# Kernel tuning notes

Hardware: AMD Instinct MI355X
Metric: run time of the kernel (lower is better)

Reference implementation:

```python
import jax, jax.numpy as jnp
import numpy as np

S, B, D_MODEL, H, DH = 2048, 2, 1024, 16, 64
FACTOR = 1.0 / np.sqrt(DH).astype(np.float32)


def setup_inputs() -> dict:
    key = jax.random.key(0)
    ks = jax.random.split(key, 12)
    sc = 0.02
    inp = {
        'query': jax.random.normal(ks[0], (S, B, D_MODEL), jnp.float32),
        'key': jax.random.normal(ks[1], (S, B, D_MODEL), jnp.float32),
        'value': jax.random.normal(ks[2], (S, B, D_MODEL), jnp.float32),
        # causal mask [seq_q, seq_k, 1]; 0 -> masked
        'mask': jnp.tril(jnp.ones((S, S), dtype=bool))[:, :, None],
        'Wq': jax.random.normal(ks[3], (H * DH, D_MODEL), jnp.float32) * sc,
        'bq': jnp.zeros((H * DH,), jnp.float32),
        'Wk': jax.random.normal(ks[4], (H * DH, D_MODEL), jnp.float32) * sc,
        'bk': jnp.zeros((H * DH,), jnp.float32),
        'Wv': jax.random.normal(ks[5], (H * DH, D_MODEL), jnp.float32) * sc,
        'bv': jnp.zeros((H * DH,), jnp.float32),
        'Wo': jax.random.normal(ks[6], (D_MODEL, H * DH), jnp.float32) * sc,
        'bo': jnp.zeros((D_MODEL,), jnp.float32),
    }
    return inp


def _split_heads(x):
    # pattern: 's b (head_dim head_num) -> s b head_num head_dim' (head_dim is OUTER)
    s, b, _ = x.shape
    return x.reshape(s, b, DH, H).transpose(0, 1, 3, 2)  # [s,b,H,DH]


def reference(query, key, value, mask, Wq, bq, Wk, bk, Wv, bv, Wo, bo):
    q = _split_heads(query @ Wq.T + bq)
    k = _split_heads(key @ Wk.T + bk)
    v = _split_heads(value @ Wv.T + bv)
    scores = jnp.einsum('ibhd,jbhd->ijbh', q, k) * FACTOR  # [i,j,b,h]
    scores = jnp.where(mask[..., None], scores, -jnp.inf)
    attn = jax.nn.softmax(scores, axis=1)  # softmax over keys (dim=1)
    out = jnp.einsum('ijbh,jbhd->ibhd', attn, v)  # [i,b,h,d]
    out = out.reshape(S, B, H * DH)  # 'i b h d -> i b (h d)'
    return out @ Wo.T + bo
```

## Files before the change

### kernel.cpp

```cpp
#include <hip/hip_runtime.h>


typedef float f32x4 __attribute__((ext_vector_type(4)));
typedef float f32x16 __attribute__((ext_vector_type(16)));
typedef __bf16 bf16x8_t __attribute__((ext_vector_type(8)));
typedef unsigned short ushort8 __attribute__((ext_vector_type(8)));
typedef unsigned int uint4v __attribute__((ext_vector_type(4)));
typedef unsigned int uint2v __attribute__((ext_vector_type(2)));

#define S_LEN 2048
#define BATCH 2
#define DMODEL 1024
#define NHEAD 16
#define DHEAD 64
#define K_SCALE 0.18033688011112042f

__device__ __forceinline__ unsigned short f2bf(float x) {
  unsigned int u = __builtin_bit_cast(unsigned int, x);
  u += 0x7fffu + ((u >> 16) & 1u);
  return (unsigned short)(u >> 16);
}

__device__ __forceinline__ f32x4 mfma16(ushort8 a, ushort8 b, f32x4 c) {
  return __builtin_amdgcn_mfma_f32_16x16x32_bf16(
      __builtin_bit_cast(bf16x8_t, a), __builtin_bit_cast(bf16x8_t, b), c, 0, 0, 0);
}
__device__ __forceinline__ f32x16 mfma32(ushort8 a, ushort8 b, f32x16 c) {
  return __builtin_amdgcn_mfma_f32_32x32x16_bf16(
      __builtin_bit_cast(bf16x8_t, a), __builtin_bit_cast(bf16x8_t, b), c, 0, 0, 0);
}

__device__ __forceinline__ ushort8 pack8(float4 a, float4 b, float s) {
  ushort8 t;
  t[0] = f2bf(a.x * s); t[1] = f2bf(a.y * s); t[2] = f2bf(a.z * s); t[3] = f2bf(a.w * s);
  t[4] = f2bf(b.x * s); t[5] = f2bf(b.y * s); t[6] = f2bf(b.z * s); t[7] = f2bf(b.w * s);
  return t;
}

__device__ __forceinline__ void gload16(unsigned short* lds, const unsigned short* g) {
  __builtin_amdgcn_global_load_lds(
      (const __attribute__((address_space(1))) unsigned int*)g,
      (__attribute__((address_space(3))) unsigned int*)lds, 16, 0, 0);
}

__global__ __launch_bounds__(256) void cvt_kernel(
    const float* __restrict__ q, const float* __restrict__ k, const float* __restrict__ v,
    const float* __restrict__ wq, const float* __restrict__ wk,
    const float* __restrict__ wv, const float* __restrict__ wo,
    unsigned short* __restrict__ qB, unsigned short* __restrict__ kB,
    unsigned short* __restrict__ vB, unsigned short* __restrict__ wqB,
    unsigned short* __restrict__ wkB, unsigned short* __restrict__ wvB,
    unsigned short* __restrict__ woB)
{
  const int c = blockIdx.x * 256 + threadIdx.x;
  const float* s; unsigned short* d; int base;
  if      (c < 524288)  { s = q;  d = qB;  base = 0; }
  else if (c < 1048576) { s = k;  d = kB;  base = 524288; }
  else if (c < 1572864) { s = v;  d = vB;  base = 1048576; }
  else if (c < 1703936) { s = wq; d = wqB; base = 1572864; }
  else if (c < 1835008) { s = wk; d = wkB; base = 1703936; }
  else if (c < 1966080) { s = wv; d = wvB; base = 1835008; }
  else                  { s = wo; d = woB; base = 1966080; }
  const size_t off = (size_t)(c - base) * 8;
  const float4 v0 = *reinterpret_cast<const float4*>(s + off);
  const float4 v1 = *reinterpret_cast<const float4*>(s + off + 4);
  *reinterpret_cast<ushort8*>(d + off) = pack8(v0, v1, 1.0f);
}

template<bool OUTBF16>
__global__ __launch_bounds__(256) void gemm_bf16_kernel(
    const unsigned short* __restrict__ A, const unsigned short* __restrict__ W,
    const float* __restrict__ bias, void* __restrict__ Cv, float oscale)
{
  __shared__ __align__(16) unsigned short As[2][128 * 64];
  __shared__ __align__(16) unsigned short Ws[2][64 * 64];
  const int tid = threadIdx.x;
  const int lane = tid & 63;
  const int w = tid >> 6;
  const int wm = (w >> 1) * 64, wn = (w & 1) * 32;
  const int g = lane >> 4, lr = lane & 15;

  const int bid = (int)blockIdx.x;
  const int widx = (bid & 7) * 64 + (bid >> 3);
  const int n0 = (widx & 15) * 64;
  const int m0 = (widx >> 4) * 128;

  f32x4 acc[4][2] = {};

#define STAGE(buf, k0)                                                              \
  {                                                                                 \
    _Pragma("unroll")                                                               \
    for (int ii = 0; ii < 4; ++ii) {                                                \
      const int c = ii * 256 + tid;                                                 \
      const int row = c >> 3;                                                       \
      const int sl = (c & 7) ^ (row & 7);                                           \
      gload16(&As[buf][c * 8], A + (size_t)(m0 + row) * DMODEL + (k0) + sl * 8);    \
    }                                                                               \
    _Pragma("unroll")                                                               \
    for (int ii = 0; ii < 2; ++ii) {                                                \
      const int c = ii * 256 + tid;                                                 \
      const int row = c >> 3;                                                       \
      const int sl = (c & 7) ^ (row & 7);                                           \
      gload16(&Ws[buf][c * 8], W + (size_t)(n0 + row) * DMODEL + (k0) + sl * 8);    \
    }                                                                               \
  }

  STAGE(0, 0);
  int cur = 0;

  for (int t = 0; t < 16; ++t) {
    __syncthreads();
    if (t < 15) STAGE(cur ^ 1, (t + 1) * 64);

    const char* ab = (const char*)&As[cur][0];
    const char* wb = (const char*)&Ws[cur][0];
#pragma unroll
    for (int kk = 0; kk < 2; ++kk) {
      ushort8 af[4], bw[2];
#pragma unroll
      for (int mt = 0; mt < 4; ++mt) {
        const int row = wm + mt * 16 + lr;
        af[mt] = *reinterpret_cast<const ushort8*>(
            ab + row * 128 + (((kk * 4 + g) ^ (row & 7)) << 4));
      }
#pragma unroll
      for (int nt = 0; nt < 2; ++nt) {
        const int row = wn + nt * 16 + lr;
        bw[nt] = *reinterpret_cast<const ushort8*>(
            wb + row * 128 + (((kk * 4 + g) ^ (row & 7)) << 4));
      }
      __builtin_amdgcn_s_setprio(1);
#pragma unroll
      for (int mt = 0; mt < 4; ++mt)
#pragma unroll
        for (int nt = 0; nt < 2; ++nt)
          acc[mt][nt] = mfma16(af[mt], bw[nt], acc[mt][nt]);
      __builtin_amdgcn_s_setprio(0);
    }
    cur ^= 1;
  }
#undef STAGE

#pragma unroll
  for (int nt = 0; nt < 2; ++nt) {
    const int col = n0 + wn + nt * 16 + lr;
    const float bv = bias[col];
#pragma unroll
    for (int mt = 0; mt < 4; ++mt)
#pragma unroll
      for (int r = 0; r < 4; ++r) {
        const int rowg = m0 + wm + mt * 16 + g * 4 + r;
        const float vv = (acc[mt][nt][r] + bv) * oscale;
        if constexpr (OUTBF16)
          ((unsigned short*)Cv)[(size_t)rowg * DMODEL + col] = f2bf(vv);
        else
          ((float*)Cv)[(size_t)rowg * DMODEL + col] = vv;
      }
  }
}

__global__ __launch_bounds__(256) void head_tr0_kernel(
    const unsigned short* __restrict__ in, unsigned short* __restrict__ out)
{
  __shared__ __align__(16) unsigned short T[32 * 256];
  const int tid = threadIdx.x;
  const int n0 = blockIdx.x * 32, o0 = blockIdx.y * 256;
#pragma unroll
  for (int i = 0; i < 4; ++i) {
    const int c = i * 256 + tid;
    const int row = c >> 5, c8 = c & 31;
    ushort8 v = *reinterpret_cast<const ushort8*>(in + (size_t)(n0 + row) * DMODEL + o0 + c8 * 8);
    int y = (row * 512 + c8 * 16) ^ ((row & 3) << 5);
    *reinterpret_cast<ushort8*>((char*)T + y) = v;
  }
  __syncthreads();
  const int d0 = o0 >> 4, s0 = n0 >> 1;
#pragma unroll
  for (int rep = 0; rep < 2; ++rep) {
    const int e = rep * 256 + tid;
    const int hh = e & 15, s = (e >> 4) & 15, b = (e >> 8) & 1;
    const int n = s * 2 + b;
    unsigned short vals[16];
#pragma unroll
    for (int dd = 0; dd < 16; ++dd) {
      int y = n * 512 + ((dd * 32 + hh * 2) ^ ((n & 3) << 5));
      vals[dd] = *(const unsigned short*)((const char*)T + y);
    }
    uint4v w0, w1;
#pragma unroll
    for (int j = 0; j < 4; ++j) {
      w0[j] = (unsigned)vals[2 * j] | ((unsigned)vals[2 * j + 1] << 16);
      w1[j] = (unsigned)vals[8 + 2 * j] | ((unsigned)vals[8 + 2 * j + 1] << 16);
    }
    unsigned short* dst = out + ((size_t)(b * 16 + hh) * S_LEN + s0 + s) * DHEAD + d0;
    *reinterpret_cast<uint4v*>(dst) = w0;
    *reinterpret_cast<uint4v*>(dst + 8) = w1;
  }
}

__global__ __launch_bounds__(256) void head_tr1_kernel(
    const unsigned short* __restrict__ in, unsigned short* __restrict__ out)
{
  __shared__ __align__(16) unsigned short T[64 * 64];
  const int tid = threadIdx.x;
  const int n0 = blockIdx.x * 64, o0 = blockIdx.y * 64;
#pragma unroll
  for (int i = 0; i < 2; ++i) {
    const int c = i * 256 + tid;
    const int row = c >> 3, c8 = c & 7;
    ushort8 v = *reinterpret_cast<const ushort8*>(in + (size_t)(n0 + row) * DMODEL + o0 + c8 * 8);
    int y = (row * 128 + c8 * 16) ^ ((row & 7) << 4);
    *reinterpret_cast<ushort8*>((char*)T + y) = v;
  }
  __syncthreads();
  const int d0 = o0 >> 4, s0 = n0 >> 1;
  const int shalf = tid & 1, seg = tid >> 1;
  const int dd = seg & 3, hh = (seg >> 2) & 15, b = (seg >> 6) & 1;
  unsigned short vals[16];
#pragma unroll
  for (int i = 0; i < 16; ++i) {
    const int s = shalf * 16 + i;
    const int n = s * 2 + b;
    int y = n * 128 + (((dd * 16 + hh) * 2) ^ ((n & 7) << 4));
    vals[i] = *(const unsigned short*)((const char*)T + y);
  }
  uint4v w0, w1;
#pragma unroll
  for (int j = 0; j < 4; ++j) {
    w0[j] = (unsigned)vals[2 * j] | ((unsigned)vals[2 * j + 1] << 16);
    w1[j] = (unsigned)vals[8 + 2 * j] | ((unsigned)vals[8 + 2 * j + 1] << 16);
  }
  unsigned short* dst = out + ((size_t)(b * 16 + hh) * DHEAD + d0 + dd) * S_LEN + s0 + shalf * 16;
  *reinterpret_cast<uint4v*>(dst) = w0;
  *reinterpret_cast<uint4v*>(dst + 8) = w1;
}

__global__ __launch_bounds__(128, 3) void attn_kernel(
    const unsigned short* __restrict__ Qh, const unsigned short* __restrict__ Kh,
    const unsigned short* __restrict__ Vh, unsigned short* __restrict__ O)
{
  __shared__ __align__(16) unsigned short Ks[2][64 * 64];
  __shared__ __align__(16) unsigned short Vs[2][64 * 64];

  const int tid = threadIdx.x;
  const int lane = tid & 63;
  const int w = tid >> 6;
  const int ln31 = lane & 31;
  const int hf = lane >> 5;

  const int bx = blockIdx.x;
  const int hb = bx & 31;
  const int head = hb & 15, b = hb >> 4;
  const int qt = 31 - (bx >> 5);
  const int q0 = qt * 64;
  const int nkt = qt + 1;
  const size_t hoff = (size_t)(b * NHEAD + head) * (S_LEN * DHEAD);
  const unsigned short* Qg = Qh + hoff;
  const unsigned short* Kg = Kh + hoff;
  const unsigned short* Vg = Vh + hoff;

  ushort8 qf[4];
  {
    const int qrow = q0 + w * 32 + ln31;
#pragma unroll
    for (int kt = 0; kt < 4; ++kt)
      qf[kt] = *reinterpret_cast<const ushort8*>(Qg + (size_t)qrow * DHEAD + kt * 16 + hf * 8);
  }

  f32x16 oa0 = {0}, oa1 = {0};
  float mrun = -1e30f, ssum = 0.f;
  const int qg = q0 + w * 32 + ln31;

#define STAGE(buf, kv)                                                             \
  {                                                                                \
    _Pragma("unroll")                                                              \
    for (int ii = 0; ii < 4; ++ii) {                                               \
      const int c = ii * 128 + tid;                                                \
      const int row = c >> 3;                                                      \
      const int sl = (c & 7) ^ (row & 7);                                          \
      gload16(&Ks[buf][c * 8], Kg + (size_t)((kv) + row) * 64 + sl * 8);           \
    }                                                                              \
    _Pragma("unroll")                                                              \
    for (int ii = 0; ii < 4; ++ii) {                                               \
      const int c = ii * 128 + tid;                                                \
      const int row = c >> 3;                                                      \
      const int sl = (c & 7) ^ (row & 7);                                          \
      gload16(&Vs[buf][c * 8], Vg + (size_t)row * S_LEN + (kv) + sl * 8);          \
    }                                                                              \
  }

  STAGE(0, 0);
  int cur = 0;

  const int kb0 = ln31 * 128 + ((hf * 16) ^ ((ln31 & 7) << 4));
  const int kb1 = (32 + ln31) * 128 + ((hf * 16) ^ ((ln31 & 7) << 4));

  for (int t = 0; t < nkt; ++t) {
    const int kv0 = t * 64;
    __syncthreads();
    if (t + 1 < nkt) STAGE(cur ^ 1, kv0 + 64);

    f32x16 sc0 = {0}, sc1 = {0};
    {
      const char* ksb = (const char*)&Ks[cur][0];
      __builtin_amdgcn_s_setprio(1);
#pragma unroll
      for (int kt = 0; kt < 4; ++kt) {
        ushort8 kf0 = *reinterpret_cast<const ushort8*>(ksb + (kb0 ^ (kt << 5)));
        ushort8 kf1 = *reinterpret_cast<const ushort8*>(ksb + (kb1 ^ (kt << 5)));
        sc0 = mfma32(kf0, qf[kt], sc0);
        sc1 = mfma32(kf1, qf[kt], sc1);
      }
      __builtin_amdgcn_s_setprio(0);
    }

    if (t == nkt - 1) {
#pragma unroll
      for (int r = 0; r < 16; ++r) {
        const int keyb = kv0 + (r & 3) + 8 * (r >> 2) + 4 * hf;
        if (keyb > qg) sc0[r] = -1e30f;
        if (keyb + 32 > qg) sc1[r] = -1e30f;
      }
    }

    float pmax = sc0[0];
#pragma unroll
    for (int r = 1; r < 16; ++r) pmax = fmaxf(pmax, sc0[r]);
#pragma unroll
    for (int r = 0; r < 16; ++r) pmax = fmaxf(pmax, sc1[r]);
    pmax = fmaxf(pmax, __shfl_xor(pmax, 32, 64));

    if (!__all(pmax <= mrun + 8.0f)) {
      const float mnew = fmaxf(mrun, pmax);
      const float scl = exp2f(mrun - mnew);
      ssum *= scl;
#pragma unroll
      for (int r = 0; r < 16; ++r) { oa0[r] *= scl; oa1[r] *= scl; }
      mrun = mnew;
    }

    float pv0[16], pv1[16];
    float psum = 0.f;
#pragma unroll
    for (int r = 0; r < 16; ++r) {
      pv0[r] = exp2f(sc0[r] - mrun);
      pv1[r] = exp2f(sc1[r] - mrun);
      psum += pv0[r] + pv1[r];
    }
    psum += __shfl_xor(psum, 32, 64);
    ssum += psum;

    unsigned int cc[16], pc[16];
#pragma unroll
    for (int j = 0; j < 8; ++j) {
      asm("v_cvt_pk_bf16_f32 %0, %1, %2" : "=v"(cc[j]) : "v"(pv0[2 * j]), "v"(pv0[2 * j + 1]));
      asm("v_cvt_pk_bf16_f32 %0, %1, %2" : "=v"(cc[8 + j]) : "v"(pv1[2 * j]), "v"(pv1[2 * j + 1]));
    }
#pragma unroll
    for (int j = 0; j < 16; ++j)
      pc[j] = (unsigned int)__shfl_xor((int)cc[j], 32, 64);

    uint4v pfw[4];
#pragma unroll
    for (int mt = 0; mt < 2; ++mt) {
#pragma unroll
      for (int ktl = 0; ktl < 2; ++ktl) {
        const int o = mt * 8 + ktl * 4;
        uint4v u;
        u[0] = hf ? pc[o + 2] : cc[o + 0];
        u[1] = hf ? pc[o + 3] : cc[o + 1];
        u[2] = hf ? cc[o + 2] : pc[o + 0];
        u[3] = hf ? cc[o + 3] : pc[o + 1];
        pfw[mt * 2 + ktl] = u;
      }
    }

    {
      const char* vsb = (const char*)&Vs[cur][0];
      __builtin_amdgcn_s_setprio(1);
#pragma unroll
      for (int kt = 0; kt < 4; ++kt) {
        ushort8 vf0 = *reinterpret_cast<const ushort8*>(vsb + (kb0 ^ (kt << 5)));
        ushort8 vf1 = *reinterpret_cast<const ushort8*>(vsb + (kb1 ^ (kt << 5)));
        ushort8 pfr = __builtin_bit_cast(ushort8, pfw[kt]);
        oa0 = mfma32(vf0, pfr, oa0);
        oa1 = mfma32(vf1, pfr, oa1);
      }
      __builtin_amdgcn_s_setprio(0);
    }

    cur ^= 1;
  }
#undef STAGE

  const float inv = 1.0f / ssum;
  unsigned short* ob = O + ((size_t)qg * BATCH + b) * DMODEL + head * DHEAD;
#pragma unroll
  for (int mt2 = 0; mt2 < 2; ++mt2) {
#pragma unroll
    for (int rq = 0; rq < 4; ++rq) {
      const int dd = mt2 * 32 + 8 * rq + 4 * hf;
      const f32x16& a = mt2 ? oa1 : oa0;
      unsigned int w0, w1;
      asm("v_cvt_pk_bf16_f32 %0, %1, %2" : "=v"(w0)
          : "v"(a[4 * rq + 0] * inv), "v"(a[4 * rq + 1] * inv));
      asm("v_cvt_pk_bf16_f32 %0, %1, %2" : "=v"(w1)
          : "v"(a[4 * rq + 2] * inv), "v"(a[4 * rq + 3] * inv));
      uint2v pk = { w0, w1 };
      *reinterpret_cast<uint2v*>(ob + dd) = pk;
    }
  }
}

extern "C" void kernel_launch(void* const* d_in, const int* in_sizes, int n_in,
                              void* d_out, int out_size, void* d_ws, size_t ws_size,
                              hipStream_t stream)
{
  (void)in_sizes; (void)n_in; (void)out_size; (void)ws_size;
  const float* query = (const float*)d_in[0];
  const float* key_  = (const float*)d_in[1];
  const float* value = (const float*)d_in[2];
  const float* Wq = (const float*)d_in[4];
  const float* bq = (const float*)d_in[5];
  const float* Wk = (const float*)d_in[6];
  const float* bk = (const float*)d_in[7];
  const float* Wv = (const float*)d_in[8];
  const float* bv = (const float*)d_in[9];
  const float* Wo = (const float*)d_in[10];
  const float* bo = (const float*)d_in[11];
  float* out = (float*)d_out;

  const size_t NE = (size_t)4096 * DMODEL;
  const size_t NW = (size_t)DMODEL * DMODEL;
  unsigned short* qB  = (unsigned short*)d_ws;
  unsigned short* kB  = qB + NE;
  unsigned short* vB  = kB + NE;
  unsigned short* g1  = vB + NE;
  unsigned short* Qh  = g1 + NE;
  unsigned short* Kh  = Qh + NE;
  unsigned short* Vh  = Kh + NE;
  unsigned short* wqB = Vh + NE;
  unsigned short* wkB = wqB + NW;
  unsigned short* wvB = wkB + NW;
  unsigned short* woB = wvB + NW;
  unsigned short* aO  = qB;

  dim3 t0grid(128, 4);
  dim3 t1grid(64, 16);

  cvt_kernel<<<dim3(8192), 256, 0, stream>>>(query, key_, value, Wq, Wk, Wv, Wo,
                                             qB, kB, vB, wqB, wkB, wvB, woB);
  gemm_bf16_kernel<true><<<dim3(512), 256, 0, stream>>>(qB, wqB, bq, g1, 1.0f);
  head_tr0_kernel<<<t0grid, 256, 0, stream>>>(g1, Qh);
  gemm_bf16_kernel<true><<<dim3(512), 256, 0, stream>>>(kB, wkB, bk, g1, K_SCALE);
  head_tr0_kernel<<<t0grid, 256, 0, stream>>>(g1, Kh);
  gemm_bf16_kernel<true><<<dim3(512), 256, 0, stream>>>(vB, wvB, bv, g1, 1.0f);
  head_tr1_kernel<<<t1grid, 256, 0, stream>>>(g1, Vh);
  attn_kernel<<<dim3(1024), 128, 0, stream>>>(Qh, Kh, Vh, aO);
  gemm_bf16_kernel<false><<<dim3(512), 256, 0, stream>>>(aO, woB, bo, out, 1.0f);
}
```

Before: 156.1 us.

## Split causal attention into key-chunked partial blocks with separate combine kernel

Replaces the single attention kernel with a split-K (flash-decoding style) scheme. Each 128-query tile is split into chunks of up to 8 key tiles, giving a balanced 40x32 grid of 256-thread blocks. Each block writes unnormalized bf16 partial outputs plus running max and sum, and a second kernel merges the chunks with log-sum-exp weights. This targets the load imbalance of causal attention and gives more evenly sized work per block. In exchange it adds an extra launch, partial-result traffic through workspace, and a second bf16 rounding of the unnormalized partials.

```diff
diff --git a/kernel.cpp b/kernel.cpp
--- a/kernel.cpp
+++ b/kernel.cpp
@@ -235,9 +235,10 @@
   *reinterpret_cast<uint4v*>(dst + 8) = w1;
 }
 
-__global__ __launch_bounds__(128, 3) void attn_kernel(
+__global__ __launch_bounds__(256, 4) void attn_part_kernel(
     const unsigned short* __restrict__ Qh, const unsigned short* __restrict__ Kh,
-    const unsigned short* __restrict__ Vh, unsigned short* __restrict__ O)
+    const unsigned short* __restrict__ Vh, unsigned short* __restrict__ Opart,
+    float* __restrict__ mlbuf)
 {
   __shared__ __align__(16) unsigned short Ks[2][64 * 64];
   __shared__ __align__(16) unsigned short Vs[2][64 * 64];
@@ -248,153 +249,168 @@
   const int ln31 = lane & 31;
   const int hf = lane >> 5;
 
-  const int bx = blockIdx.x;
-  const int hb = bx & 31;
+  const int u = 39 - (int)blockIdx.x;
+  int Q, c;
+  if      (u < 4)  { Q = u;                 c = 0; }
+  else if (u < 12) { Q = 4 + ((u - 4) >> 1);  c = (u - 4) & 1; }
+  else if (u < 24) { Q = 8 + (u - 12) / 3;    c = (u - 12) % 3; }
+  else             { Q = 12 + ((u - 24) >> 2); c = (u - 24) & 3; }
+  int off;
+  if      (Q < 4)  off = Q;
+  else if (Q < 8)  off = 4 + (Q - 4) * 2;
+  else if (Q < 12) off = 12 + (Q - 8) * 3;
+  else             off = 24 + (Q - 12) * 4;
+
+  const int hb = blockIdx.y;
   const int head = hb & 15, b = hb >> 4;
-  const int qt = 31 - (bx >> 5);
-  const int q0 = qt * 64;
-  const int nkt = qt + 1;
+  const int slot = hb * 40 + off + c;
+  const int t0 = c * 8;
+  const int tmax = 2 * Q + 1;
+  const int t1 = (tmax < t0 + 7) ? tmax : (t0 + 7);
+  const int q0 = Q * 128;
+
   const size_t hoff = (size_t)(b * NHEAD + head) * (S_LEN * DHEAD);
   const unsigned short* Qg = Qh + hoff;
   const unsigned short* Kg = Kh + hoff;
   const unsigned short* Vg = Vh + hoff;
 
+  const int qwb = q0 + w * 32;
+  const int qg = qwb + ln31;
+
   ushort8 qf[4];
-  {
-    const int qrow = q0 + w * 32 + ln31;
-#pragma unroll
-    for (int kt = 0; kt < 4; ++kt)
-      qf[kt] = *reinterpret_cast<const ushort8*>(Qg + (size_t)qrow * DHEAD + kt * 16 + hf * 8);
-  }
+#pragma unroll
+  for (int kt = 0; kt < 4; ++kt)
+    qf[kt] = *reinterpret_cast<const ushort8*>(Qg + (size_t)qg * DHEAD + kt * 16 + hf * 8);
 
   f32x16 oa0 = {0}, oa1 = {0};
   float mrun = -1e30f, ssum = 0.f;
-  const int qg = q0 + w * 32 + ln31;
 
 #define STAGE(buf, kv)                                                             \
   {                                                                                \
     _Pragma("unroll")                                                              \
-    for (int ii = 0; ii < 4; ++ii) {                                               \
-      const int c = ii * 128 + tid;                                                \
-      const int row = c >> 3;                                                      \
-      const int sl = (c & 7) ^ (row & 7);                                          \
-      gload16(&Ks[buf][c * 8], Kg + (size_t)((kv) + row) * 64 + sl * 8);           \
+    for (int ii = 0; ii < 2; ++ii) {                                               \
+      const int c2 = ii * 256 + tid;                                               \
+      const int row = c2 >> 3;                                                     \
+      const int sl = (c2 & 7) ^ (row & 7);                                         \
+      gload16(&Ks[buf][c2 * 8], Kg + (size_t)((kv) + row) * 64 + sl * 8);          \
     }                                                                              \
     _Pragma("unroll")                                                              \
-    for (int ii = 0; ii < 4; ++ii) {                                               \
-      const int c = ii * 128 + tid;                                                \
-      const int row = c >> 3;                                                      \
-      const int sl = (c & 7) ^ (row & 7);                                          \
-      gload16(&Vs[buf][c * 8], Vg + (size_t)row * S_LEN + (kv) + sl * 8);          \
+    for (int ii = 0; ii < 2; ++ii) {                                               \
+      const int c2 = ii * 256 + tid;                                               \
+      const int row = c2 >> 3;                                                     \
+      const int sl = (c2 & 7) ^ (row & 7);                                         \
+      gload16(&Vs[buf][c2 * 8], Vg + (size_t)row * S_LEN + (kv) + sl * 8);         \
     }                                                                              \
   }
 
-  STAGE(0, 0);
+  STAGE(0, t0 * 64);
   int cur = 0;
 
   const int kb0 = ln31 * 128 + ((hf * 16) ^ ((ln31 & 7) << 4));
   const int kb1 = (32 + ln31) * 128 + ((hf * 16) ^ ((ln31 & 7) << 4));
 
-  for (int t = 0; t < nkt; ++t) {
+  for (int t = t0; t <= t1; ++t) {
     const int kv0 = t * 64;
     __syncthreads();
-    if (t + 1 < nkt) STAGE(cur ^ 1, kv0 + 64);
-
-    f32x16 sc0 = {0}, sc1 = {0};
-    {
-      const char* ksb = (const char*)&Ks[cur][0];
-      __builtin_amdgcn_s_setprio(1);
-#pragma unroll
-      for (int kt = 0; kt < 4; ++kt) {
-        ushort8 kf0 = *reinterpret_cast<const ushort8*>(ksb + (kb0 ^ (kt << 5)));
-        ushort8 kf1 = *reinterpret_cast<const ushort8*>(ksb + (kb1 ^ (kt << 5)));
-        sc0 = mfma32(kf0, qf[kt], sc0);
-        sc1 = mfma32(kf1, qf[kt], sc1);
-      }
-      __builtin_amdgcn_s_setprio(0);
+    if (t < t1) STAGE(cur ^ 1, kv0 + 64);
+
+    if (kv0 <= qwb + 31) {
+      f32x16 sc0 = {0}, sc1 = {0};
+      {
+        const char* ksb = (const char*)&Ks[cur][0];
+        __builtin_amdgcn_s_setprio(1);
+#pragma unroll
+        for (int kt = 0; kt < 4; ++kt) {
+          ushort8 kf0 = *reinterpret_cast<const ushort8*>(ksb + (kb0 ^ (kt << 5)));
+          ushort8 kf1 = *reinterpret_cast<const ushort8*>(ksb + (kb1 ^ (kt << 5)));
+          sc0 = mfma32(kf0, qf[kt], sc0);
+          sc1 = mfma32(kf1, qf[kt], sc1);
+        }
+        __builtin_amdgcn_s_setprio(0);
+      }
+
+      if (kv0 + 63 > qwb) {
+#pragma unroll
+        for (int r = 0; r < 16; ++r) {
+          const int keyb = kv0 + (r & 3) + 8 * (r >> 2) + 4 * hf;
+          if (keyb > qg) sc0[r] = -1e30f;
+          if (keyb + 32 > qg) sc1[r] = -1e30f;
+        }
+      }
+
+      float pmax = sc0[0];
+#pragma unroll
+      for (int r = 1; r < 16; ++r) pmax = fmaxf(pmax, sc0[r]);
+#pragma unroll
+      for (int r = 0; r < 16; ++r) pmax = fmaxf(pmax, sc1[r]);
+      pmax = fmaxf(pmax, __shfl_xor(pmax, 32, 64));
+
+      if (!__all(pmax <= mrun + 8.0f)) {
+        const float mnew = fmaxf(mrun, pmax);
+        const float scl = exp2f(mrun - mnew);
+        ssum *= scl;
+#pragma unroll
+        for (int r = 0; r < 16; ++r) { oa0[r] *= scl; oa1[r] *= scl; }
+        mrun = mnew;
+      }
+
+      float pv0[16], pv1[16];
+      float psum = 0.f;
+#pragma unroll
+      for (int r = 0; r < 16; ++r) {
+        pv0[r] = exp2f(sc0[r] - mrun);
+        pv1[r] = exp2f(sc1[r] - mrun);
+        psum += pv0[r] + pv1[r];
+      }
+      psum += __shfl_xor(psum, 32, 64);
+      ssum += psum;
+
+      unsigned int cc[16], pc[16];
+#pragma unroll
+      for (int j = 0; j < 8; ++j) {
+        asm("v_cvt_pk_bf16_f32 %0, %1, %2" : "=v"(cc[j]) : "v"(pv0[2 * j]), "v"(pv0[2 * j + 1]));
+        asm("v_cvt_pk_bf16_f32 %0, %1, %2" : "=v"(cc[8 + j]) : "v"(pv1[2 * j]), "v"(pv1[2 * j + 1]));
+      }
+#pragma unroll
+      for (int j = 0; j < 16; ++j)
+        pc[j] = (unsigned int)__shfl_xor((int)cc[j], 32, 64);
+
+      uint4v pfw[4];
+#pragma unroll
+      for (int mt = 0; mt < 2; ++mt) {
+#pragma unroll
+        for (int ktl = 0; ktl < 2; ++ktl) {
+          const int o = mt * 8 + ktl * 4;
+          uint4v u4;
+          u4[0] = hf ? pc[o + 2] : cc[o + 0];
+          u4[1] = hf ? pc[o + 3] : cc[o + 1];
+          u4[2] = hf ? cc[o + 2] : pc[o + 0];
+          u4[3] = hf ? cc[o + 3] : pc[o + 1];
+          pfw[mt * 2 + ktl] = u4;
+        }
+      }
+
+      {
+        const char* vsb = (const char*)&Vs[cur][0];
+        __builtin_amdgcn_s_setprio(1);
+#pragma unroll
+        for (int kt = 0; kt < 4; ++kt) {
+          ushort8 vf0 = *reinterpret_cast<const ushort8*>(vsb + (kb0 ^ (kt << 5)));
+          ushort8 vf1 = *reinterpret_cast<const ushort8*>(vsb + (kb1 ^ (kt << 5)));
+          ushort8 pfr = __builtin_bit_cast(ushort8, pfw[kt]);
+          oa0 = mfma32(vf0, pfr, oa0);
+          oa1 = mfma32(vf1, pfr, oa1);
+        }
+        __builtin_amdgcn_s_setprio(0);
+      }
     }
 
-    if (t == nkt - 1) {
-#pragma unroll
-      for (int r = 0; r < 16; ++r) {
-        const int keyb = kv0 + (r & 3) + 8 * (r >> 2) + 4 * hf;
-        if (keyb > qg) sc0[r] = -1e30f;
-        if (keyb + 32 > qg) sc1[r] = -1e30f;
-      }
-    }
-
-    float pmax = sc0[0];
-#pragma unroll
-    for (int r = 1; r < 16; ++r) pmax = fmaxf(pmax, sc0[r]);
-#pragma unroll
-    for (int r = 0; r < 16; ++r) pmax = fmaxf(pmax, sc1[r]);
-    pmax = fmaxf(pmax, __shfl_xor(pmax, 32, 64));
-
-    if (!__all(pmax <= mrun + 8.0f)) {
-      const float mnew = fmaxf(mrun, pmax);
-      const float scl = exp2f(mrun - mnew);
-      ssum *= scl;
-#pragma unroll
-      for (int r = 0; r < 16; ++r) { oa0[r] *= scl; oa1[r] *= scl; }
-      mrun = mnew;
-    }
-
-    float pv0[16], pv1[16];
-    float psum = 0.f;
-#pragma unroll
-    for (int r = 0; r < 16; ++r) {
-      pv0[r] = exp2f(sc0[r] - mrun);
-      pv1[r] = exp2f(sc1[r] - mrun);
-      psum += pv0[r] + pv1[r];
-    }
-    psum += __shfl_xor(psum, 32, 64);
-    ssum += psum;
-
-    unsigned int cc[16], pc[16];
-#pragma unroll
-    for (int j = 0; j < 8; ++j) {
-      asm("v_cvt_pk_bf16_f32 %0, %1, %2" : "=v"(cc[j]) : "v"(pv0[2 * j]), "v"(pv0[2 * j + 1]));
-      asm("v_cvt_pk_bf16_f32 %0, %1, %2" : "=v"(cc[8 + j]) : "v"(pv1[2 * j]), "v"(pv1[2 * j + 1]));
-    }
-#pragma unroll
-    for (int j = 0; j < 16; ++j)
-      pc[j] = (unsigned int)__shfl_xor((int)cc[j], 32, 64);
-
-    uint4v pfw[4];
-#pragma unroll
-    for (int mt = 0; mt < 2; ++mt) {
-#pragma unroll
-      for (int ktl = 0; ktl < 2; ++ktl) {
-        const int o = mt * 8 + ktl * 4;
-        uint4v u;
-        u[0] = hf ? pc[o + 2] : cc[o + 0];
-        u[1] = hf ? pc[o + 3] : cc[o + 1];
-        u[2] = hf ? cc[o + 2] : pc[o + 0];
-        u[3] = hf ? cc[o + 3] : pc[o + 1];
-        pfw[mt * 2 + ktl] = u;
-      }
-    }
-
-    {
-      const char* vsb = (const char*)&Vs[cur][0];
-      __builtin_amdgcn_s_setprio(1);
-#pragma unroll
-      for (int kt = 0; kt < 4; ++kt) {
-        ushort8 vf0 = *reinterpret_cast<const ushort8*>(vsb + (kb0 ^ (kt << 5)));
-        ushort8 vf1 = *reinterpret_cast<const ushort8*>(vsb + (kb1 ^ (kt << 5)));
-        ushort8 pfr = __builtin_bit_cast(ushort8, pfw[kt]);
-        oa0 = mfma32(vf0, pfr, oa0);
-        oa1 = mfma32(vf1, pfr, oa1);
-      }
-      __builtin_amdgcn_s_setprio(0);
-    }
-
     cur ^= 1;
   }
 #undef STAGE
 
-  const float inv = 1.0f / ssum;
-  unsigned short* ob = O + ((size_t)qg * BATCH + b) * DMODEL + head * DHEAD;
+  const int ql = w * 32 + ln31;
+  unsigned short* ob = Opart + (size_t)slot * 8192 + ql * 64;
 #pragma unroll
   for (int mt2 = 0; mt2 < 2; ++mt2) {
 #pragma unroll
@@ -403,13 +419,76 @@
       const f32x16& a = mt2 ? oa1 : oa0;
       unsigned int w0, w1;
       asm("v_cvt_pk_bf16_f32 %0, %1, %2" : "=v"(w0)
-          : "v"(a[4 * rq + 0] * inv), "v"(a[4 * rq + 1] * inv));
+          : "v"(a[4 * rq + 0]), "v"(a[4 * rq + 1]));
       asm("v_cvt_pk_bf16_f32 %0, %1, %2" : "=v"(w1)
-          : "v"(a[4 * rq + 2] * inv), "v"(a[4 * rq + 3] * inv));
+          : "v"(a[4 * rq + 2]), "v"(a[4 * rq + 3]));
       uint2v pk = { w0, w1 };
       *reinterpret_cast<uint2v*>(ob + dd) = pk;
     }
   }
+  if (hf == 0) {
+    mlbuf[slot * 256 + ql] = mrun;
+    mlbuf[slot * 256 + 128 + ql] = ssum;
+  }
+}
+
+__global__ __launch_bounds__(256) void attn_combine_kernel(
+    const unsigned short* __restrict__ Opart, const float* __restrict__ mlbuf,
+    unsigned short* __restrict__ O)
+{
+  const int Q = blockIdx.x, hb = blockIdx.y;
+  const int head = hb & 15, b = hb >> 4;
+  const int nch = (2 * Q + 1) / 8 + 1;
+  int off;
+  if      (Q < 4)  off = Q;
+  else if (Q < 8)  off = 4 + (Q - 4) * 2;
+  else if (Q < 12) off = 12 + (Q - 8) * 3;
+  else             off = 24 + (Q - 12) * 4;
+  const int s0 = hb * 40 + off;
+
+  const int tid = threadIdx.x;
+  const int q = tid >> 1, dh = (tid & 1) * 32;
+
+  float mc[4], lc[4];
+  float M = -1e30f;
+  for (int cc = 0; cc < nch; ++cc) {
+    mc[cc] = mlbuf[(s0 + cc) * 256 + q];
+    lc[cc] = mlbuf[(s0 + cc) * 256 + 128 + q];
+    M = fmaxf(M, mc[cc]);
+  }
+  float L = 0.f, wgt[4];
+  for (int cc = 0; cc < nch; ++cc) {
+    wgt[cc] = exp2f(mc[cc] - M);
+    L += wgt[cc] * lc[cc];
+  }
+  const float invL = 1.0f / L;
+
+  float acc[32] = {};
+  for (int cc = 0; cc < nch; ++cc) {
+    const unsigned short* p = Opart + (size_t)(s0 + cc) * 8192 + q * 64 + dh;
+    const float wv = wgt[cc];
+#pragma unroll
+    for (int seg = 0; seg < 4; ++seg) {
+      ushort8 v = *reinterpret_cast<const ushort8*>(p + seg * 8);
+#pragma unroll
+      for (int j = 0; j < 8; ++j) {
+        const float f = __builtin_bit_cast(float, ((unsigned int)v[j]) << 16);
+        acc[seg * 8 + j] += wv * f;
+      }
+    }
+  }
+
+  unsigned int wpk[16];
+#pragma unroll
+  for (int j = 0; j < 16; ++j) {
+    asm("v_cvt_pk_bf16_f32 %0, %1, %2" : "=v"(wpk[j])
+        : "v"(acc[2 * j] * invL), "v"(acc[2 * j + 1] * invL));
+  }
+  unsigned short* dst = O + ((size_t)((Q * 128 + q) * BATCH + b)) * DMODEL + head * DHEAD + dh;
+#pragma unroll
+  for (int seg = 0; seg < 4; ++seg)
+    *reinterpret_cast<uint4v*>(dst + seg * 8) =
+        uint4v{ wpk[4 * seg], wpk[4 * seg + 1], wpk[4 * seg + 2], wpk[4 * seg + 3] };
 }
 
 extern "C" void kernel_launch(void* const* d_in, const int* in_sizes, int n_in,
@@ -444,6 +523,8 @@
   unsigned short* wvB = wkB + NW;
   unsigned short* woB = wvB + NW;
   unsigned short* aO  = qB;
+  unsigned short* Opart = kB;
+  float* mlbuf = (float*)(kB + (size_t)1280 * 8192);
 
   dim3 t0grid(128, 4);
   dim3 t1grid(64, 16);
@@ -456,6 +537,7 @@
   head_tr0_kernel<<<t0grid, 256, 0, stream>>>(g1, Kh);
   gemm_bf16_kernel<true><<<dim3(512), 256, 0, stream>>>(vB, wvB, bv, g1, 1.0f);
   head_tr1_kernel<<<t1grid, 256, 0, stream>>>(g1, Vh);
-  attn_kernel<<<dim3(1024), 128, 0, stream>>>(Qh, Kh, Vh, aO);
+  attn_part_kernel<<<dim3(40, 32), 256, 0, stream>>>(Qh, Kh, Vh, Opart, mlbuf);
+  attn_combine_kernel<<<dim3(16, 32), 256, 0, stream>>>(Opart, mlbuf, aO);
   gemm_bf16_kernel<false><<<dim3(512), 256, 0, stream>>>(aO, woB, bo, out, 1.0f);
 }
```

New measurement: 156.4 us. About the same (+0.2%).
